# Kernel tuning notes

Measured on AMD Instinct MI355X. Metric: run time of the kernel, lower is better.

Reference implementation:

```python
import jax, jax.numpy as jnp
import numpy as np

PROJ_DIM = 8192
INPUT_DIM = 512
THRESH = 1e-08


def _signed_sqrt(x):
    return jnp.sign(x) * jnp.sqrt(jnp.abs(x))


def _make_sketch_matrix(key, input_dim, proj_dim):
    kh, ks = jax.random.split(key)
    h = jax.random.randint(kh, (input_dim,), 0, proj_dim)
    s = jnp.sign(jax.random.uniform(ks, (input_dim,), minval=-1.0, maxval=1.0)).astype(jnp.float32)
    M = jnp.zeros((input_dim, proj_dim), dtype=jnp.float32)
    return M.at[jnp.arange(input_dim), h].set(s)


def setup_inputs() -> dict:
    key = jax.random.key(0)
    kx, k1, k2 = jax.random.split(key, 3)
    x = jax.random.normal(kx, (32, 14, 14, INPUT_DIM), dtype=jnp.float32)
    M1 = _make_sketch_matrix(k1, INPUT_DIM, PROJ_DIM)
    M2 = _make_sketch_matrix(k2, INPUT_DIM, PROJ_DIM)
    return {"x": x, "M1": M1, "M2": M2}


def reference(x, M1, M2):
    B, H, W, C = x.shape
    x_flat = x.reshape(-1, C)                      # [B*H*W, C]
    # count-sketch projections (dense matmul, as in the original layer)
    p1 = (x_flat @ M1).astype(jnp.complex64)       # [B*H*W, P]
    p2 = (x_flat @ M2).astype(jnp.complex64)
    # circular convolution via FFT
    sketch = jnp.fft.fft(p1, axis=-1) * jnp.fft.fft(p2, axis=-1)
    y = jnp.real(jnp.fft.ifft(sketch, axis=-1)).astype(jnp.float32)
    y = y.reshape(B, H, W, -1).sum(axis=(1, 2))    # sum-pool over spatial dims -> [B, P]
    y = _signed_sqrt(y)
    # tf.nn.l2_normalize(x, axis=1, epsilon=1e-10)
    inv_norm = jax.lax.rsqrt(jnp.maximum(jnp.sum(y * y, axis=1, keepdims=True), 1e-10))
    return y * inv_norm
```

## Files before the change

### kernel.cpp

```cpp
#include <hip/hip_runtime.h>
#include <math.h>

#define PROJ 8192
#define CDIM 512
#define HWPOS 196
#define NBATCH 32
#define NSLAB 7
#define NTP 10

typedef __attribute__((ext_vector_type(8))) short   short8;
typedef __attribute__((ext_vector_type(4))) float   f32x4;

__device__ __forceinline__ unsigned short f2bf(float f) {
    unsigned u = __float_as_uint(f);
    u += 0x7fff + ((u >> 16) & 1);
    return (unsigned short)(u >> 16);
}
__device__ __forceinline__ float bf2f(unsigned short h) {
    return __uint_as_float(((unsigned)h) << 16);
}

__device__ __forceinline__ void lds_fadd(float* p, float v) {
    __attribute__((address_space(3))) float* lp =
        (__attribute__((address_space(3))) float*)p;
    asm volatile("ds_add_f32 %0, %1" : : "v"(lp), "v"(v) : "memory");
}

__global__ __launch_bounds__(256) void extract_kernel(
    const float* __restrict__ M1, const float* __restrict__ M2,
    int* __restrict__ h1, float* __restrict__ s1,
    int* __restrict__ h2, float* __restrict__ s2,
    float* __restrict__ norm)
{
    const int row = blockIdx.x;
    const float* M = blockIdx.y ? M2 : M1;
    int*   h = blockIdx.y ? h2 : h1;
    float* s = blockIdx.y ? s2 : s1;
    const float* mrow = M + (size_t)row * PROJ;

    if (blockIdx.x == 0 && blockIdx.y == 0 && threadIdx.x < NBATCH)
        norm[threadIdx.x] = 0.0f;

    for (int i = threadIdx.x * 4; i < PROJ; i += 256 * 4) {
        float4 v = *(const float4*)(mrow + i);
        if (v.x != 0.0f) { h[row] = i + 0; s[row] = v.x; }
        if (v.y != 0.0f) { h[row] = i + 1; s[row] = v.y; }
        if (v.z != 0.0f) { h[row] = i + 2; s[row] = v.z; }
        if (v.w != 0.0f) { h[row] = i + 3; s[row] = v.w; }
    }
}

__global__ __launch_bounds__(256) void prep_kernel(
    const float* __restrict__ x,
    unsigned short* __restrict__ XThi, unsigned short* __restrict__ XTlo)
{
    const int ks  = blockIdx.x;
    const int bat = blockIdx.y;
    const int tid = threadIdx.x;
    __shared__ float xt[32][513];

    const float* xb = x + (size_t)bat * HWPOS * CDIM;
    const int k0 = ks * 32;
#pragma unroll
    for (int i = 0; i < 16; ++i) {
        const int idx = i * 1024 + tid * 4;
        const int kr  = idx >> 9;
        const int c   = idx & 511;
        float4 v = make_float4(0.f, 0.f, 0.f, 0.f);
        if (k0 + kr < HWPOS) v = *(const float4*)(xb + (size_t)(k0 + kr) * CDIM + c);
        xt[kr][c+0] = v.x; xt[kr][c+1] = v.y; xt[kr][c+2] = v.z; xt[kr][c+3] = v.w;
    }
    __syncthreads();

    unsigned short* ohi = XThi + ((size_t)bat * NSLAB + ks) * 16384;
    unsigned short* olo = XTlo + ((size_t)bat * NSLAB + ks) * 16384;
#pragma unroll
    for (int i = 0; i < 8; ++i) {
        const int ch   = i * 256 + tid;
        const int c16  = ch & 15;
        const int quad = (ch >> 4) & 3;
        const int cgrp = ch >> 6;
        const int c    = cgrp * 16 + c16;
        short8 vh, vl;
#pragma unroll
        for (int j = 0; j < 8; ++j) {
            float f = xt[quad * 8 + j][c];
            unsigned short h = f2bf(f);
            vh[j] = (short)h;
            vl[j] = (short)f2bf(f - bf2f(h));
        }
        *(short8*)(ohi + ch * 8) = vh;
        *(short8*)(olo + ch * 8) = vl;
    }
}

__global__ __launch_bounds__(256) void gramscatter_kernel(
    const unsigned short* __restrict__ XThi, const unsigned short* __restrict__ XTlo,
    const int* __restrict__ h1, const float* __restrict__ s1,
    const int* __restrict__ h2, const float* __restrict__ s2,
    float* __restrict__ pbins)
{
    const int id  = blockIdx.x;
    const int sub = id >> 3;
    const int tp  = sub % NTP;
    const int bat = (id & 7) + 8 * (sub / NTP);
    const int bi  = (tp < 4) ? 0 : (tp < 7) ? 1 : (tp < 9) ? 2 : 3;
    const int bj  = (tp < 4) ? tp : (tp < 7) ? (tp - 3) : (tp < 9) ? (tp - 5) : 3;
    const int tid  = threadIdx.x;
    const int w    = tid >> 6;
    const int lane = tid & 63;

    __shared__ __align__(16) unsigned short Sbuf[2][4][4096];
    __shared__ float bins[PROJ];
    __shared__ int   th1[256]; __shared__ float ts1[256];
    __shared__ int   th2[256]; __shared__ float ts2[256];

    const int tile = (w < 2) ? bi : bj;
    const unsigned short* srcbase = ((w & 1) ? XTlo : XThi)
                                  + (size_t)bat * NSLAB * 16384 + (size_t)tile * 4096;
    const int rowq = w >> 1, colq = w & 1;

    {
        const unsigned short* src = srcbase;
        unsigned short* dst = &Sbuf[0][w][0];
#pragma unroll
        for (int i = 0; i < 8; ++i)
            __builtin_amdgcn_global_load_lds(
                (const __attribute__((address_space(1))) void*)(src + i * 512 + lane * 8),
                (__attribute__((address_space(3))) void*)(dst + i * 512), 16, 0, 0);
    }

    for (int i = tid; i < PROJ; i += 256) bins[i] = 0.f;
    {
        const int g = (tid < 128) ? (bi * 128 + tid) : (bj * 128 + tid - 128);
        th1[tid] = h1[g]; ts1[tid] = s1[g];
        th2[tid] = h2[g]; ts2[tid] = s2[g];
    }

    f32x4 acc[16];
#pragma unroll
    for (int i = 0; i < 16; ++i) { acc[i][0]=0.f; acc[i][1]=0.f; acc[i][2]=0.f; acc[i][3]=0.f; }

    for (int ks = 0; ks < NSLAB; ++ks) {
        __syncthreads();
        const int buf = ks & 1;

        if (ks + 1 < NSLAB) {
            const unsigned short* src = srcbase + (size_t)(ks + 1) * 16384;
            unsigned short* dst = &Sbuf[buf ^ 1][w][0];
#pragma unroll
            for (int i = 0; i < 8; ++i)
                __builtin_amdgcn_global_load_lds(
                    (const __attribute__((address_space(1))) void*)(src + i * 512 + lane * 8),
                    (__attribute__((address_space(3))) void*)(dst + i * 512), 16, 0, 0);
        }

        short8 ah[4], al[4], bh[4], bl[4];
#pragma unroll
        for (int t = 0; t < 4; ++t) {
            ah[t] = *(const short8*)&Sbuf[buf][0][(rowq * 4 + t) * 512 + lane * 8];
            al[t] = *(const short8*)&Sbuf[buf][1][(rowq * 4 + t) * 512 + lane * 8];
            bh[t] = *(const short8*)&Sbuf[buf][2][(colq * 4 + t) * 512 + lane * 8];
            bl[t] = *(const short8*)&Sbuf[buf][3][(colq * 4 + t) * 512 + lane * 8];
        }
#pragma unroll
        for (int mt = 0; mt < 4; ++mt)
#pragma unroll
            for (int nt = 0; nt < 4; ++nt) {
                const int idx = mt * 4 + nt;
                acc[idx] = __builtin_amdgcn_mfma_f32_16x16x32_bf16(ah[mt], bh[nt], acc[idx], 0, 0, 0);
                acc[idx] = __builtin_amdgcn_mfma_f32_16x16x32_bf16(ah[mt], bl[nt], acc[idx], 0, 0, 0);
                acc[idx] = __builtin_amdgcn_mfma_f32_16x16x32_bf16(al[mt], bh[nt], acc[idx], 0, 0, 0);
            }
    }

    const bool mirror = (bi != bj);
    int   h2c[4], h1c[4];
    float s2c[4], s1c[4];
#pragma unroll
    for (int nt = 0; nt < 4; ++nt) {
        const int cl = colq * 64 + nt * 16 + (lane & 15);
        h2c[nt] = th2[128 + cl]; s2c[nt] = ts2[128 + cl];
        h1c[nt] = th1[128 + cl]; s1c[nt] = ts1[128 + cl];
    }
    const int quad = lane >> 4;
#pragma unroll
    for (int mt = 0; mt < 4; ++mt)
#pragma unroll
        for (int reg = 0; reg < 4; ++reg) {
            const int rl = rowq * 64 + mt * 16 + quad * 4 + reg;
            const int   h1r = th1[rl]; const float s1r = ts1[rl];
            const int   h2r = th2[rl]; const float s2r = ts2[rl];
#pragma unroll
            for (int nt = 0; nt < 4; ++nt) {
                const float v = acc[mt * 4 + nt][reg];
                lds_fadd(&bins[(h1r + h2c[nt]) & (PROJ - 1)], s1r * s2c[nt] * v);
                if (mirror)
                    lds_fadd(&bins[(h1c[nt] + h2r) & (PROJ - 1)], s1c[nt] * s2r * v);
            }
        }
    __syncthreads();

    float* dst = pbins + ((size_t)bat * NTP + tp) * PROJ;
    for (int i = tid * 4; i < PROJ; i += 1024)
        *(float4*)(dst + i) = *(const float4*)&bins[i];
}

__global__ __launch_bounds__(256) void reduce_kernel(
    const float* __restrict__ pbins, float* __restrict__ out,
    float* __restrict__ norm)
{
    const int chunk = blockIdx.x;
    const int bat   = blockIdx.y;
    const int tid   = threadIdx.x;
    const int base  = chunk * 1024 + tid * 4;

    const float* pb = pbins + (size_t)bat * NTP * PROJ;
    float4 v = make_float4(0.f, 0.f, 0.f, 0.f);
#pragma unroll
    for (int t = 0; t < NTP; ++t) {
        float4 p = *(const float4*)(pb + (size_t)t * PROJ + base);
        v.x += p.x; v.y += p.y; v.z += p.z; v.w += p.w;
    }

    float4 sv;
    sv.x = (v.x >= 0.f) ? sqrtf(v.x) : -sqrtf(-v.x);
    sv.y = (v.y >= 0.f) ? sqrtf(v.y) : -sqrtf(-v.y);
    sv.z = (v.z >= 0.f) ? sqrtf(v.z) : -sqrtf(-v.z);
    sv.w = (v.w >= 0.f) ? sqrtf(v.w) : -sqrtf(-v.w);
    *(float4*)(out + (size_t)bat * PROJ + base) = sv;

    float local = fabsf(v.x) + fabsf(v.y) + fabsf(v.z) + fabsf(v.w);
#pragma unroll
    for (int off = 32; off > 0; off >>= 1) local += __shfl_down(local, off, 64);

    __shared__ float wred[4];
    if ((tid & 63) == 0) wred[tid >> 6] = local;
    __syncthreads();
    if (tid == 0)
        unsafeAtomicAdd(&norm[bat], wred[0] + wred[1] + wred[2] + wred[3]);
}

__global__ __launch_bounds__(256) void normalize_kernel(
    float* __restrict__ out, const float* __restrict__ norm)
{
    const int bat = blockIdx.y;
    const int idx = blockIdx.x * 1024 + threadIdx.x * 4;
    const float inv = rsqrtf(fmaxf(norm[bat], 1e-10f));
    float4* p = (float4*)(out + (size_t)bat * PROJ + idx);
    float4 v = *p;
    v.x *= inv; v.y *= inv; v.z *= inv; v.w *= inv;
    *p = v;
}

extern "C" void kernel_launch(void* const* d_in, const int* in_sizes, int n_in,
                              void* d_out, int out_size, void* d_ws, size_t ws_size,
                              hipStream_t stream)
{
    const float* x  = (const float*)d_in[0];
    const float* M1 = (const float*)d_in[1];
    const float* M2 = (const float*)d_in[2];
    float* out = (float*)d_out;

    char* ws = (char*)d_ws;
    int*            h1    = (int*)   (ws + 0);
    float*          s1    = (float*) (ws + 2048);
    int*            h2    = (int*)   (ws + 4096);
    float*          s2    = (float*) (ws + 6144);
    float*          norm  = (float*) (ws + 8192);
    unsigned short* XThi  = (unsigned short*)(ws + 16384);
    unsigned short* XTlo  = (unsigned short*)(ws + 7356416);
    float*          pbins = (float*) (ws + 14696448);

    extract_kernel<<<dim3(512, 2), 256, 0, stream>>>(M1, M2, h1, s1, h2, s2, norm);
    prep_kernel<<<dim3(NSLAB, NBATCH), 256, 0, stream>>>(x, XThi, XTlo);
    gramscatter_kernel<<<NTP * NBATCH, 256, 0, stream>>>(XThi, XTlo, h1, s1, h2, s2, pbins);
    reduce_kernel<<<dim3(8, NBATCH), 256, 0, stream>>>(pbins, out, norm);
    normalize_kernel<<<dim3(8, NBATCH), 256, 0, stream>>>(out, norm);
}
```

Baseline: 185.3 us.

## Rebalance gram tiles into 8 equal-work units and fuse reduce with normalize

The 10 tile-pairs per batch become 8 work units of equal cost. Each of the two units covering diagonal tiles processes two diagonal tiles in sequence, and each of the other six handles one off-diagonal tile together with its mirror scatter. This gives 256 blocks instead of 320, which could fill one wave on 256 CUs, and it shrinks the partial-bin pages from 10 to 8 per batch. The reduce and normalize kernels merge into a single 512-thread block per batch, which removes a launch and the global atomic norm. The cost is that the finalize step runs on only 32 blocks, and the diagonal units run serially with an extra sync.

```diff
diff --git a/kernel.cpp b/kernel.cpp
--- a/kernel.cpp
+++ b/kernel.cpp
@@ -6,7 +6,8 @@
 #define HWPOS 196
 #define NBATCH 32
 #define NSLAB 7
-#define NTP 10
+#define NUNITF 8
+#define NPAGES 8
 
 typedef __attribute__((ext_vector_type(8))) short   short8;
 typedef __attribute__((ext_vector_type(4))) float   f32x4;
@@ -102,52 +103,42 @@
 {
     const int id  = blockIdx.x;
     const int sub = id >> 3;
-    const int tp  = sub % NTP;
-    const int bat = (id & 7) + 8 * (sub / NTP);
-    const int bi  = (tp < 4) ? 0 : (tp < 7) ? 1 : (tp < 9) ? 2 : 3;
-    const int bj  = (tp < 4) ? tp : (tp < 7) ? (tp - 3) : (tp < 9) ? (tp - 5) : 3;
+    const int u   = sub & 7;
+    const int bat = (id & 7) + 8 * (sub >> 3);
+    const bool pair  = (u < 2);
+    const bool doMir = (u >= 2);
+    const int  k6    = u - 2;
+
     const int tid  = threadIdx.x;
     const int w    = tid >> 6;
     const int lane = tid & 63;
+    const int rowq = w >> 1, colq = w & 1;
 
     __shared__ __align__(16) unsigned short Sbuf[2][4][4096];
     __shared__ float bins[PROJ];
     __shared__ int   th1[256]; __shared__ float ts1[256];
     __shared__ int   th2[256]; __shared__ float ts2[256];
 
-    const int tile = (w < 2) ? bi : bj;
-    const unsigned short* srcbase = ((w & 1) ? XTlo : XThi)
-                                  + (size_t)bat * NSLAB * 16384 + (size_t)tile * 4096;
-    const int rowq = w >> 1, colq = w & 1;
-
-    {
-        const unsigned short* src = srcbase;
-        unsigned short* dst = &Sbuf[0][w][0];
-#pragma unroll
-        for (int i = 0; i < 8; ++i)
-            __builtin_amdgcn_global_load_lds(
-                (const __attribute__((address_space(1))) void*)(src + i * 512 + lane * 8),
-                (__attribute__((address_space(3))) void*)(dst + i * 512), 16, 0, 0);
-    }
-
     for (int i = tid; i < PROJ; i += 256) bins[i] = 0.f;
-    {
-        const int g = (tid < 128) ? (bi * 128 + tid) : (bj * 128 + tid - 128);
-        th1[tid] = h1[g]; ts1[tid] = s1[g];
-        th2[tid] = h2[g]; ts2[tid] = s2[g];
-    }
-
-    f32x4 acc[16];
-#pragma unroll
-    for (int i = 0; i < 16; ++i) { acc[i][0]=0.f; acc[i][1]=0.f; acc[i][2]=0.f; acc[i][3]=0.f; }
-
-    for (int ks = 0; ks < NSLAB; ++ks) {
-        __syncthreads();
-        const int buf = ks & 1;
-
-        if (ks + 1 < NSLAB) {
-            const unsigned short* src = srcbase + (size_t)(ks + 1) * 16384;
-            unsigned short* dst = &Sbuf[buf ^ 1][w][0];
+
+    for (int rep = 0; rep < 2; ++rep) {
+        if (rep == 1 && !pair) break;
+        const int bi = pair ? (2 * u + rep) : (int)((0x211000u >> (k6 * 4)) & 15);
+        const int bj = pair ? (2 * u + rep) : (int)((0x332321u >> (k6 * 4)) & 15);
+
+        {
+            const int g = (tid < 128) ? (bi * 128 + tid) : (bj * 128 + tid - 128);
+            th1[tid] = h1[g]; ts1[tid] = s1[g];
+            th2[tid] = h2[g]; ts2[tid] = s2[g];
+        }
+
+        const int tile = (w < 2) ? bi : bj;
+        const unsigned short* srcbase = ((w & 1) ? XTlo : XThi)
+                                      + (size_t)bat * NSLAB * 16384 + (size_t)tile * 4096;
+
+        {
+            const unsigned short* src = srcbase;
+            unsigned short* dst = &Sbuf[0][w][0];
 #pragma unroll
             for (int i = 0; i < 8; ++i)
                 __builtin_amdgcn_global_load_lds(
@@ -155,102 +146,126 @@
                     (__attribute__((address_space(3))) void*)(dst + i * 512), 16, 0, 0);
         }
 
-        short8 ah[4], al[4], bh[4], bl[4];
-#pragma unroll
-        for (int t = 0; t < 4; ++t) {
-            ah[t] = *(const short8*)&Sbuf[buf][0][(rowq * 4 + t) * 512 + lane * 8];
-            al[t] = *(const short8*)&Sbuf[buf][1][(rowq * 4 + t) * 512 + lane * 8];
-            bh[t] = *(const short8*)&Sbuf[buf][2][(colq * 4 + t) * 512 + lane * 8];
-            bl[t] = *(const short8*)&Sbuf[buf][3][(colq * 4 + t) * 512 + lane * 8];
-        }
+        f32x4 acc[16];
+#pragma unroll
+        for (int i = 0; i < 16; ++i) { acc[i][0]=0.f; acc[i][1]=0.f; acc[i][2]=0.f; acc[i][3]=0.f; }
+
+        for (int ks = 0; ks < NSLAB; ++ks) {
+            __syncthreads();
+            const int buf = ks & 1;
+
+            if (ks + 1 < NSLAB) {
+                const unsigned short* src = srcbase + (size_t)(ks + 1) * 16384;
+                unsigned short* dst = &Sbuf[buf ^ 1][w][0];
+#pragma unroll
+                for (int i = 0; i < 8; ++i)
+                    __builtin_amdgcn_global_load_lds(
+                        (const __attribute__((address_space(1))) void*)(src + i * 512 + lane * 8),
+                        (__attribute__((address_space(3))) void*)(dst + i * 512), 16, 0, 0);
+            }
+
+            short8 ah[4], al[4], bh[4], bl[4];
+#pragma unroll
+            for (int t = 0; t < 4; ++t) {
+                ah[t] = *(const short8*)&Sbuf[buf][0][(rowq * 4 + t) * 512 + lane * 8];
+                al[t] = *(const short8*)&Sbuf[buf][1][(rowq * 4 + t) * 512 + lane * 8];
+                bh[t] = *(const short8*)&Sbuf[buf][2][(colq * 4 + t) * 512 + lane * 8];
+                bl[t] = *(const short8*)&Sbuf[buf][3][(colq * 4 + t) * 512 + lane * 8];
+            }
+#pragma unroll
+            for (int mt = 0; mt < 4; ++mt)
+#pragma unroll
+                for (int nt = 0; nt < 4; ++nt) {
+                    const int idx = mt * 4 + nt;
+                    acc[idx] = __builtin_amdgcn_mfma_f32_16x16x32_bf16(ah[mt], bh[nt], acc[idx], 0, 0, 0);
+                    acc[idx] = __builtin_amdgcn_mfma_f32_16x16x32_bf16(ah[mt], bl[nt], acc[idx], 0, 0, 0);
+                    acc[idx] = __builtin_amdgcn_mfma_f32_16x16x32_bf16(al[mt], bh[nt], acc[idx], 0, 0, 0);
+                }
+        }
+
+        int   h2c[4], h1c[4];
+        float s2c[4], s1c[4];
+#pragma unroll
+        for (int nt = 0; nt < 4; ++nt) {
+            const int cl = colq * 64 + nt * 16 + (lane & 15);
+            h2c[nt] = th2[128 + cl]; s2c[nt] = ts2[128 + cl];
+            h1c[nt] = th1[128 + cl]; s1c[nt] = ts1[128 + cl];
+        }
+        const int quad = lane >> 4;
 #pragma unroll
         for (int mt = 0; mt < 4; ++mt)
 #pragma unroll
-            for (int nt = 0; nt < 4; ++nt) {
-                const int idx = mt * 4 + nt;
-                acc[idx] = __builtin_amdgcn_mfma_f32_16x16x32_bf16(ah[mt], bh[nt], acc[idx], 0, 0, 0);
-                acc[idx] = __builtin_amdgcn_mfma_f32_16x16x32_bf16(ah[mt], bl[nt], acc[idx], 0, 0, 0);
-                acc[idx] = __builtin_amdgcn_mfma_f32_16x16x32_bf16(al[mt], bh[nt], acc[idx], 0, 0, 0);
+            for (int reg = 0; reg < 4; ++reg) {
+                const int rl = rowq * 64 + mt * 16 + quad * 4 + reg;
+                const int   h1r = th1[rl]; const float s1r = ts1[rl];
+                const int   h2r = th2[rl]; const float s2r = ts2[rl];
+#pragma unroll
+                for (int nt = 0; nt < 4; ++nt) {
+                    const float v = acc[mt * 4 + nt][reg];
+                    lds_fadd(&bins[(h1r + h2c[nt]) & (PROJ - 1)], s1r * s2c[nt] * v);
+                    if (doMir)
+                        lds_fadd(&bins[(h1c[nt] + h2r) & (PROJ - 1)], s1c[nt] * s2r * v);
+                }
             }
-    }
-
-    const bool mirror = (bi != bj);
-    int   h2c[4], h1c[4];
-    float s2c[4], s1c[4];
-#pragma unroll
-    for (int nt = 0; nt < 4; ++nt) {
-        const int cl = colq * 64 + nt * 16 + (lane & 15);
-        h2c[nt] = th2[128 + cl]; s2c[nt] = ts2[128 + cl];
-        h1c[nt] = th1[128 + cl]; s1c[nt] = ts1[128 + cl];
-    }
-    const int quad = lane >> 4;
-#pragma unroll
-    for (int mt = 0; mt < 4; ++mt)
-#pragma unroll
-        for (int reg = 0; reg < 4; ++reg) {
-            const int rl = rowq * 64 + mt * 16 + quad * 4 + reg;
-            const int   h1r = th1[rl]; const float s1r = ts1[rl];
-            const int   h2r = th2[rl]; const float s2r = ts2[rl];
-#pragma unroll
-            for (int nt = 0; nt < 4; ++nt) {
-                const float v = acc[mt * 4 + nt][reg];
-                lds_fadd(&bins[(h1r + h2c[nt]) & (PROJ - 1)], s1r * s2c[nt] * v);
-                if (mirror)
-                    lds_fadd(&bins[(h1c[nt] + h2r) & (PROJ - 1)], s1c[nt] * s2r * v);
-            }
-        }
-    __syncthreads();
-
-    float* dst = pbins + ((size_t)bat * NTP + tp) * PROJ;
+        __syncthreads();
+    }
+
+    float* dst = pbins + ((size_t)bat * NPAGES + u) * PROJ;
     for (int i = tid * 4; i < PROJ; i += 1024)
         *(float4*)(dst + i) = *(const float4*)&bins[i];
 }
 
-__global__ __launch_bounds__(256) void reduce_kernel(
-    const float* __restrict__ pbins, float* __restrict__ out,
-    float* __restrict__ norm)
-{
-    const int chunk = blockIdx.x;
-    const int bat   = blockIdx.y;
-    const int tid   = threadIdx.x;
-    const int base  = chunk * 1024 + tid * 4;
-
-    const float* pb = pbins + (size_t)bat * NTP * PROJ;
-    float4 v = make_float4(0.f, 0.f, 0.f, 0.f);
-#pragma unroll
-    for (int t = 0; t < NTP; ++t) {
-        float4 p = *(const float4*)(pb + (size_t)t * PROJ + base);
-        v.x += p.x; v.y += p.y; v.z += p.z; v.w += p.w;
-    }
-
-    float4 sv;
-    sv.x = (v.x >= 0.f) ? sqrtf(v.x) : -sqrtf(-v.x);
-    sv.y = (v.y >= 0.f) ? sqrtf(v.y) : -sqrtf(-v.y);
-    sv.z = (v.z >= 0.f) ? sqrtf(v.z) : -sqrtf(-v.z);
-    sv.w = (v.w >= 0.f) ? sqrtf(v.w) : -sqrtf(-v.w);
-    *(float4*)(out + (size_t)bat * PROJ + base) = sv;
-
-    float local = fabsf(v.x) + fabsf(v.y) + fabsf(v.z) + fabsf(v.w);
+__global__ __launch_bounds__(512) void finalize_kernel(
+    const float* __restrict__ pbins, float* __restrict__ out)
+{
+    const int bat = blockIdx.x;
+    const int tid = threadIdx.x;
+    const float* pb = pbins + (size_t)bat * NPAGES * PROJ;
+
+    float4 y0, y1, y2, y3;
+    float local = 0.f;
+
+#pragma unroll
+    for (int c = 0; c < 4; ++c) {
+        const int base = c * 2048 + tid * 4;
+        float4 a = make_float4(0.f, 0.f, 0.f, 0.f);
+#pragma unroll
+        for (int t = 0; t < NPAGES; ++t) {
+            float4 p = *(const float4*)(pb + (size_t)t * PROJ + base);
+            a.x += p.x; a.y += p.y; a.z += p.z; a.w += p.w;
+        }
+        local += fabsf(a.x) + fabsf(a.y) + fabsf(a.z) + fabsf(a.w);
+        float4 sv;
+        sv.x = (a.x >= 0.f) ? sqrtf(a.x) : -sqrtf(-a.x);
+        sv.y = (a.y >= 0.f) ? sqrtf(a.y) : -sqrtf(-a.y);
+        sv.z = (a.z >= 0.f) ? sqrtf(a.z) : -sqrtf(-a.z);
+        sv.w = (a.w >= 0.f) ? sqrtf(a.w) : -sqrtf(-a.w);
+        if (c == 0) y0 = sv; else if (c == 1) y1 = sv; else if (c == 2) y2 = sv; else y3 = sv;
+    }
+
 #pragma unroll
     for (int off = 32; off > 0; off >>= 1) local += __shfl_down(local, off, 64);
 
-    __shared__ float wred[4];
+    __shared__ float wred[8];
+    __shared__ float sinv;
     if ((tid & 63) == 0) wred[tid >> 6] = local;
     __syncthreads();
-    if (tid == 0)
-        unsafeAtomicAdd(&norm[bat], wred[0] + wred[1] + wred[2] + wred[3]);
-}
-
-__global__ __launch_bounds__(256) void normalize_kernel(
-    float* __restrict__ out, const float* __restrict__ norm)
-{
-    const int bat = blockIdx.y;
-    const int idx = blockIdx.x * 1024 + threadIdx.x * 4;
-    const float inv = rsqrtf(fmaxf(norm[bat], 1e-10f));
-    float4* p = (float4*)(out + (size_t)bat * PROJ + idx);
-    float4 v = *p;
-    v.x *= inv; v.y *= inv; v.z *= inv; v.w *= inv;
-    *p = v;
+    if (tid == 0) {
+        float t = 0.f;
+#pragma unroll
+        for (int i = 0; i < 8; ++i) t += wred[i];
+        sinv = rsqrtf(fmaxf(t, 1e-10f));
+    }
+    __syncthreads();
+    const float inv = sinv;
+
+    float* ob = out + (size_t)bat * PROJ;
+#pragma unroll
+    for (int c = 0; c < 4; ++c) {
+        float4 sv = (c == 0) ? y0 : (c == 1) ? y1 : (c == 2) ? y2 : y3;
+        sv.x *= inv; sv.y *= inv; sv.z *= inv; sv.w *= inv;
+        *(float4*)(ob + c * 2048 + tid * 4) = sv;
+    }
 }
 
 extern "C" void kernel_launch(void* const* d_in, const int* in_sizes, int n_in,
@@ -274,7 +289,6 @@
 
     extract_kernel<<<dim3(512, 2), 256, 0, stream>>>(M1, M2, h1, s1, h2, s2, norm);
     prep_kernel<<<dim3(NSLAB, NBATCH), 256, 0, stream>>>(x, XThi, XTlo);
-    gramscatter_kernel<<<NTP * NBATCH, 256, 0, stream>>>(XThi, XTlo, h1, s1, h2, s2, pbins);
-    reduce_kernel<<<dim3(8, NBATCH), 256, 0, stream>>>(pbins, out, norm);
-    normalize_kernel<<<dim3(8, NBATCH), 256, 0, stream>>>(out, norm);
-}
+    gramscatter_kernel<<<NUNITF * NBATCH, 256, 0, stream>>>(XThi, XTlo, h1, s1, h2, s2, pbins);
+    finalize_kernel<<<NBATCH, 512, 0, stream>>>(pbins, out);
+}
```

Result: faster. 161.2 us (-13.0%).
